# Performance work log

Hardware: AMD Instinct MI355X
Metric: run time of the kernel (lower is better)

## Reference

```python
import jax, jax.numpy as jnp
import numpy as np

B, C, N, H = 4, 256, 1024, 8
D = C // H
EPS = 1e-5

def setup_inputs() -> dict:
    key = jax.random.key(0)
    ks = jax.random.split(key, 10)
    s = lambda k, shape: (jax.random.normal(k, shape, jnp.float32) * 0.02)
    return dict(
        node_embeds=jax.random.normal(ks[0], (B, C, N), jnp.float32),
        edge_embeds=jax.random.normal(ks[1], (B, N, N), jnp.float32),
        da_prior=jax.random.normal(ks[2], (B, N, C), jnp.float32),
        gamma=jnp.ones((C,), jnp.float32),
        beta=jnp.zeros((C,), jnp.float32),
        w_qkv=s(ks[3], (C, 3 * C)),            # Linear(node_dim, 3*node_dim), no bias
        w_proj=s(ks[4], (C, C)),
        b_proj=jnp.zeros((C,), jnp.float32),
        w_expand=s(ks[5], (H,)),               # Conv2d(1,H,1) weight (per-head scalar)
        b_expand=jnp.zeros((H,), jnp.float32),
        w_reduce=s(ks[6], (H,)),               # Conv2d(H,1,1) weight
        b_reduce=jnp.zeros((1,), jnp.float32),
        w_fc=s(ks[7], (1, C)),                 # Linear(edge_dim=1, node_dim)
        b_fc=jnp.zeros((C,), jnp.float32),
    )

def reference(node_embeds, edge_embeds, da_prior, gamma, beta, w_qkv,
              w_proj, b_proj, w_expand, b_expand, w_reduce, b_reduce, w_fc, b_fc):
    x = jnp.swapaxes(node_embeds, 1, 2)                       # [B,N,C]
    # einsum 'bnn,bnc->bnc': diagonal of edge matrix scales each node
    diag = jnp.diagonal(edge_embeds, axis1=1, axis2=2)        # [B,N]
    attned = diag[:, :, None] * x                             # [B,N,C]
    # einsum 'bnc,bca->bnc' with prior permuted [B,C,A]: multiply by sum over A
    prior_sum = da_prior.sum(axis=1)                          # [B,C]
    x = attned * prior_sum[:, None, :] + x                    # residual add
    # LayerNorm over channel dim
    mu = x.mean(-1, keepdims=True)
    var = x.var(-1, keepdims=True)
    ln = (x - mu) * jax.lax.rsqrt(var + EPS) * gamma + beta
    qkv = (ln @ w_qkv).reshape(B, N, 3, H, D)
    q = jnp.transpose(qkv[:, :, 0], (0, 2, 1, 3))             # [B,H,N,D]
    k = jnp.transpose(qkv[:, :, 1], (0, 2, 1, 3))
    v = jnp.transpose(qkv[:, :, 2], (0, 2, 1, 3))
    scale = D ** -0.5
    attn = jnp.einsum('bhnd,bhmd->bhnm', q, k) * scale        # [B,H,N,N]
    bias = edge_embeds[:, None] * w_expand[None, :, None, None] + b_expand[None, :, None, None]
    attn = attn + bias                                        # pre-softmax scores = residual
    a = jax.nn.softmax(attn, axis=-1)
    node = jnp.einsum('bhnm,bhmd->bnhd', a, v).reshape(B, N, C)
    # reduce conv over heads on (softmax + residual)
    edge = jnp.einsum('bhnm,h->bnm', a + attn, w_reduce) + b_reduce[0]  # [B,N,N]
    w = jax.nn.softmax(edge, axis=-1)
    wsum = (w * edge).sum(-1)                                 # [B,N]
    node = node + wsum[:, :, None] @ w_fc + b_fc              # fc: [B,N,1]@[1,C]
    node = node @ w_proj + b_proj
    return jnp.swapaxes(node, 1, 2), edge                     # ([B,C,N], [B,N,N])
```

## Files before the change

kernel.cpp:

```cpp
#include <hip/hip_runtime.h>
#include <math.h>

#define Bn 4
#define Cn 256
#define Nn 1024
#define Hn 8
#define Dn 32
#define BHND (Bn * Hn * Nn * Dn)
#define BHN  (Bn * Hn * Nn)

typedef short bf16x8 __attribute__((ext_vector_type(8)));
typedef float f32x4 __attribute__((ext_vector_type(4)));

__device__ inline unsigned f2bf_rn_bits(float x) {
  union { float f; unsigned u; } v; v.f = x;
  return (v.u + 0x7FFFu + ((v.u >> 16) & 1u)) >> 16;
}
__device__ inline float bfbits2f(unsigned b) {
  union { unsigned u; float f; } v; v.u = b << 16; return v.f;
}
__device__ inline void split_bf(float x, unsigned& hi, unsigned& lo) {
  hi = f2bf_rn_bits(x);
  lo = f2bf_rn_bits(x - bfbits2f(hi));
}
__device__ inline unsigned split_bf_trunc_pack(float x) {
  union { float f; unsigned u; } v; v.f = x;
  unsigned hi = v.u >> 16;
  union { unsigned u; float f; } hv; hv.u = hi << 16;
  union { float f; unsigned u; } r; r.f = x - hv.f;
  return hi | (r.u & 0xffff0000u);
}
__device__ inline void split4(const float4& a, float sc, short4& hs, short4& ls) {
  unsigned hb, lb;
  split_bf(a.x * sc, hb, lb); hs.x = (short)hb; ls.x = (short)lb;
  split_bf(a.y * sc, hb, lb); hs.y = (short)hb; ls.y = (short)lb;
  split_bf(a.z * sc, hb, lb); hs.z = (short)hb; ls.z = (short)lb;
  split_bf(a.w * sc, hb, lb); hs.w = (short)hb; ls.w = (short)lb;
}
__device__ inline void unpack_u32x8(const uint4& a, const uint4& b, bf16x8& hi, bf16x8& lo) {
  int4 h4, l4;
  h4.x = (int)((a.x & 0xffffu) | (a.y << 16));  l4.x = (int)((a.x >> 16) | (a.y & 0xffff0000u));
  h4.y = (int)((a.z & 0xffffu) | (a.w << 16));  l4.y = (int)((a.z >> 16) | (a.w & 0xffff0000u));
  h4.z = (int)((b.x & 0xffffu) | (b.y << 16));  l4.z = (int)((b.x >> 16) | (b.y & 0xffff0000u));
  h4.w = (int)((b.z & 0xffffu) | (b.w << 16));  l4.w = (int)((b.z >> 16) | (b.w & 0xffff0000u));
  hi = *(bf16x8*)&h4; lo = *(bf16x8*)&l4;
}

__global__ __launch_bounds__(256) void k_prior_part(const float* __restrict__ dap,
                                                    float* __restrict__ pp) {
  int bi = blockIdx.x;
  int b = bi >> 5, ch = bi & 31;
  int c = threadIdx.x;
  float s = 0.f;
  int n0 = ch * 32;
  for (int n = n0; n < n0 + 32; ++n) s += dap[(size_t)(b * Nn + n) * Cn + c];
  pp[(size_t)(b * 32 + ch) * Cn + c] = s;
}

__global__ __launch_bounds__(256) void k_prior_red(const float* __restrict__ pp,
                                                   float* __restrict__ prior) {
  int i = blockIdx.x * 256 + threadIdx.x;
  int b = i >> 8, c = i & 255;
  float s = 0.f;
  for (int ch = 0; ch < 32; ++ch) s += pp[(size_t)(b * 32 + ch) * Cn + c];
  prior[i] = s;
}

__global__ __launch_bounds__(256) void k_prep_ln(const float* __restrict__ ne,
                                                 const float* __restrict__ eg,
                                                 const float* __restrict__ prior,
                                                 const float* __restrict__ gamma,
                                                 const float* __restrict__ beta,
                                                 float* __restrict__ ln) {
  int blk = blockIdx.x;
  int xcd = blk & 7, idx = blk >> 3;
  int b = idx >> 7;
  int n = xcd * 128 + (idx & 127);
  int c = threadIdx.x;
  float x = ne[(size_t)(b * Cn + c) * Nn + n];
  float dg = eg[(size_t)(b * Nn + n) * Nn + n];
  float x2 = x * (1.f + dg * prior[b * Cn + c]);
  float s = x2, qq = x2 * x2;
#pragma unroll
  for (int off = 32; off >= 1; off >>= 1) {
    s += __shfl_xor(s, off);
    qq += __shfl_xor(qq, off);
  }
  __shared__ float ss[4], sq[4];
  if ((c & 63) == 0) { ss[c >> 6] = s; sq[c >> 6] = qq; }
  __syncthreads();
  s = ss[0] + ss[1] + ss[2] + ss[3];
  qq = sq[0] + sq[1] + sq[2] + sq[3];
  float mu = s * (1.f / 256.f);
  float var = qq * (1.f / 256.f) - mu * mu;
  float r = rsqrtf(var + 1e-5f);
  ln[(size_t)(b * Nn + n) * Cn + c] = (x2 - mu) * r * gamma[c] + beta[c];
}

__global__ __launch_bounds__(256) void k_qkv_gemm(const float* __restrict__ ln,
                                                  const float* __restrict__ wqkv,
                                                  short* __restrict__ q_hi,
                                                  short* __restrict__ q_lo,
                                                  short* __restrict__ k_hi,
                                                  short* __restrict__ k_lo,
                                                  short* __restrict__ vt_hi,
                                                  short* __restrict__ vt_lo) {
  __shared__ __align__(16) float at[16][68];
  __shared__ __align__(16) float bt[16][68];
  __shared__ float ct[64][65];
  int m0 = blockIdx.x * 64;
  int j0 = blockIdx.y * 64;
  int t = threadIdx.x;
  int tx = t & 15, ty = t >> 4;
  float4 acc[4] = {};
  for (int k0 = 0; k0 < 256; k0 += 16) {
    {
      int row = t >> 2, k4 = (t & 3) << 2;
      float4 a = *(const float4*)&ln[(size_t)(m0 + row) * 256 + k0 + k4];
      at[k4 + 0][row] = a.x; at[k4 + 1][row] = a.y;
      at[k4 + 2][row] = a.z; at[k4 + 3][row] = a.w;
      int rb = t >> 4, jb = (t & 15) << 2;
      *(float4*)&bt[rb][jb] = *(const float4*)&wqkv[(size_t)(k0 + rb) * 768 + j0 + jb];
    }
    __syncthreads();
#pragma unroll
    for (int kk = 0; kk < 16; ++kk) {
      float4 a4 = *(float4*)&at[kk][ty << 2];
      float4 b4 = *(float4*)&bt[kk][tx << 2];
      acc[0].x += a4.x * b4.x; acc[0].y += a4.x * b4.y; acc[0].z += a4.x * b4.z; acc[0].w += a4.x * b4.w;
      acc[1].x += a4.y * b4.x; acc[1].y += a4.y * b4.y; acc[1].z += a4.y * b4.z; acc[1].w += a4.y * b4.w;
      acc[2].x += a4.z * b4.x; acc[2].y += a4.z * b4.y; acc[2].z += a4.z * b4.z; acc[2].w += a4.z * b4.w;
      acc[3].x += a4.w * b4.x; acc[3].y += a4.w * b4.y; acc[3].z += a4.w * b4.z; acc[3].w += a4.w * b4.w;
    }
    __syncthreads();
  }
  int b = m0 >> 10, n0 = m0 & 1023;
  int three = (j0 + (tx << 2)) >> 8;
  const float scale = 0.17677669529663687f;
  if (three == 2) {
#pragma unroll
    for (int i = 0; i < 4; ++i) {
      ct[(ty << 2) + i][(tx << 2) + 0] = acc[i].x;
      ct[(ty << 2) + i][(tx << 2) + 1] = acc[i].y;
      ct[(ty << 2) + i][(tx << 2) + 2] = acc[i].z;
      ct[(ty << 2) + i][(tx << 2) + 3] = acc[i].w;
    }
    __syncthreads();
    int jl = t >> 2;
    int n4 = (t & 3) * 16;
    int rem = (j0 & 255) + jl;
    int h = rem >> 5, d = rem & 31;
    short hs[16], ls[16];
#pragma unroll
    for (int u = 0; u < 16; ++u) {
      unsigned hb, lb;
      split_bf(ct[n4 + u][jl], hb, lb);
      hs[u] = (short)hb; ls[u] = (short)lb;
    }
    size_t ob = ((size_t)(b * Hn + h) * Dn + d) * Nn + n0 + n4;
    *(uint4*)&vt_hi[ob] = *(uint4*)&hs[0];
    *(uint4*)&vt_hi[ob + 8] = *(uint4*)&hs[8];
    *(uint4*)&vt_lo[ob] = *(uint4*)&ls[0];
    *(uint4*)&vt_lo[ob + 8] = *(uint4*)&ls[8];
  } else {
    int j = j0 + (tx << 2);
    int rem = j & 255, h = rem >> 5, dd = rem & 31;
    short* dst_hi = (three == 0) ? q_hi : k_hi;
    short* dst_lo = (three == 0) ? q_lo : k_lo;
    float sc = (three == 0) ? 1.0f : scale;
#pragma unroll
    for (int i = 0; i < 4; ++i) {
      int m = m0 + (ty << 2) + i;
      int bb = m >> 10, n = m & 1023;
      size_t base = (size_t)((bb * Hn + h) * Nn + n) * Dn + dd;
      short4 hs, ls; split4(acc[i], sc, hs, ls);
      *(short4*)&dst_hi[base] = hs; *(short4*)&dst_lo[base] = ls;
    }
  }
}

__global__ __launch_bounds__(256, 4) void k_attn_core(
    const short* __restrict__ q_hi, const short* __restrict__ q_lo,
    const short* __restrict__ k_hi, const short* __restrict__ k_lo,
    const short* __restrict__ vt_hi, const short* __restrict__ vt_lo,
    const float* __restrict__ eg,
    const float* __restrict__ w_expand, const float* __restrict__ b_expand,
    float* __restrict__ o_part, float* __restrict__ l_part) {
  __shared__ short kh[64 * 40];
  __shared__ short kl[64 * 40];
  __shared__ short vth[32 * 72];
  __shared__ short vtl[32 * 72];
  __shared__ unsigned pbuf[4][16 * 68];

  int blk = blockIdx.x;
  int mh = blk & 1;
  int nt = (blk >> 1) & 15;
  int h = (blk >> 5) & 7;
  int b = blk >> 8;
  int n0 = nt * 64;
  int t = threadIdx.x, wid = t >> 6, l = t & 63;
  int lr = l & 15, lq = l >> 4;

  const float we = w_expand[h], be = b_expand[h];
  size_t bhb = (size_t)(b * Hn + h) * Nn * Dn;
  const short* khg = k_hi + bhb;
  const short* klg = k_lo + bhb;
  const short* vhg = vt_hi + bhb;
  const short* vlg = vt_lo + bhb;

  bf16x8 qhi, qlo;
  {
    size_t qoff = bhb + (size_t)(n0 + wid * 16 + lr) * Dn + lq * 8;
    qhi = *(const bf16x8*)&q_hi[qoff];
    qlo = *(const bf16x8*)&q_lo[qoff];
  }

  f32x4 O0 = {0.f, 0.f, 0.f, 0.f}, O1 = {0.f, 0.f, 0.f, 0.f};
  float rowsum[4] = {0.f, 0.f, 0.f, 0.f};
  int nrow = n0 + wid * 16 + lq * 4;

  for (int ms = 0; ms < 8; ++ms) {
    int m0 = mh * 512 + ms * 64;
    float eb[4][4];
#pragma unroll
    for (int reg = 0; reg < 4; ++reg) {
      const float* ep = &eg[(size_t)(b * Nn + nrow + reg) * Nn + m0 + lr];
#pragma unroll
      for (int msub = 0; msub < 4; ++msub) eb[msub][reg] = ep[msub * 16];
    }
    __syncthreads();
    {
      int row = t >> 2, c = (t & 3) * 8;
      *(uint4*)&kh[row * 40 + c] = *(const uint4*)&khg[(size_t)(m0 + row) * Dn + c];
      *(uint4*)&kl[row * 40 + c] = *(const uint4*)&klg[(size_t)(m0 + row) * Dn + c];
      int d = t >> 3, cm = (t & 7) * 8;
      *(uint4*)&vth[d * 72 + cm] = *(const uint4*)&vhg[(size_t)d * Nn + m0 + cm];
      *(uint4*)&vtl[d * 72 + cm] = *(const uint4*)&vlg[(size_t)d * Nn + m0 + cm];
    }
    __syncthreads();

#pragma unroll
    for (int msub = 0; msub < 4; ++msub) {
      int mrow = msub * 16 + lr;
      bf16x8 bh8 = *(bf16x8*)&kh[mrow * 40 + lq * 8];
      bf16x8 bl8 = *(bf16x8*)&kl[mrow * 40 + lq * 8];
      f32x4 sacc = {0.f, 0.f, 0.f, 0.f};
      sacc = __builtin_amdgcn_mfma_f32_16x16x32_bf16(qlo, bh8, sacc, 0, 0, 0);
      sacc = __builtin_amdgcn_mfma_f32_16x16x32_bf16(qhi, bl8, sacc, 0, 0, 0);
      sacc = __builtin_amdgcn_mfma_f32_16x16x32_bf16(qhi, bh8, sacc, 0, 0, 0);
#pragma unroll
      for (int reg = 0; reg < 4; ++reg) {
        float s = sacc[reg] + eb[msub][reg] * we + be;
        float e = __expf(s);
        rowsum[reg] += e;
        pbuf[wid][(lq * 4 + reg) * 68 + msub * 16 + lr] = split_bf_trunc_pack(e);
      }
    }

#pragma unroll
    for (int mw = 0; mw < 2; ++mw) {
      uint4 pa = *(uint4*)&pbuf[wid][lr * 68 + mw * 32 + lq * 8];
      uint4 pb = *(uint4*)&pbuf[wid][lr * 68 + mw * 32 + lq * 8 + 4];
      bf16x8 ahi, alo;
      unpack_u32x8(pa, pb, ahi, alo);
      {
        bf16x8 vh8 = *(bf16x8*)&vth[lr * 72 + mw * 32 + lq * 8];
        bf16x8 vl8 = *(bf16x8*)&vtl[lr * 72 + mw * 32 + lq * 8];
        O0 = __builtin_amdgcn_mfma_f32_16x16x32_bf16(alo, vh8, O0, 0, 0, 0);
        O0 = __builtin_amdgcn_mfma_f32_16x16x32_bf16(ahi, vl8, O0, 0, 0, 0);
        O0 = __builtin_amdgcn_mfma_f32_16x16x32_bf16(ahi, vh8, O0, 0, 0, 0);
      }
      {
        bf16x8 vh8 = *(bf16x8*)&vth[(16 + lr) * 72 + mw * 32 + lq * 8];
        bf16x8 vl8 = *(bf16x8*)&vtl[(16 + lr) * 72 + mw * 32 + lq * 8];
        O1 = __builtin_amdgcn_mfma_f32_16x16x32_bf16(alo, vh8, O1, 0, 0, 0);
        O1 = __builtin_amdgcn_mfma_f32_16x16x32_bf16(ahi, vl8, O1, 0, 0, 0);
        O1 = __builtin_amdgcn_mfma_f32_16x16x32_bf16(ahi, vh8, O1, 0, 0, 0);
      }
    }
  }

#pragma unroll
  for (int reg = 0; reg < 4; ++reg) {
#pragma unroll
    for (int off = 1; off < 16; off <<= 1)
      rowsum[reg] += __shfl_xor(rowsum[reg], off);
  }
  size_t pbase = (size_t)mh * BHND + bhb;
#pragma unroll
  for (int reg = 0; reg < 4; ++reg) {
    int n = nrow + reg;
    o_part[pbase + (size_t)n * Dn + lr] = O0[reg];
    o_part[pbase + (size_t)n * Dn + 16 + lr] = O1[reg];
    if (lr == 0)
      l_part[(size_t)mh * BHN + (size_t)(b * Hn + h) * Nn + n] = rowsum[reg];
  }
}

__global__ __launch_bounds__(256, 4) void k_edge_mfma(
    const short* __restrict__ q_hi, const short* __restrict__ q_lo,
    const short* __restrict__ k_hi, const short* __restrict__ k_lo,
    const float* __restrict__ eg, const float* __restrict__ l_part,
    const float* __restrict__ w_expand, const float* __restrict__ b_expand,
    const float* __restrict__ w_reduce, const float* __restrict__ b_reduce,
    float* __restrict__ edge_out) {
  __shared__ short kh[64 * 40];
  __shared__ short kl[64 * 40];
  int blk = blockIdx.x;
  int mt = blk & 15;
  int nt = (blk >> 4) & 15;
  int b = blk >> 8;
  int n0 = nt * 64, m0 = mt * 64;
  int t = threadIdx.x, wid = t >> 6, l = t & 63;
  int lr = l & 15, lq = l >> 4;
  const float br = b_reduce[0];
  int nrow = n0 + wid * 16 + lq * 4;

  float eacc[4][4], ebias[4][4];
#pragma unroll
  for (int reg = 0; reg < 4; ++reg) {
    const float* ep = &eg[(size_t)(b * Nn + nrow + reg) * Nn + m0 + lr];
#pragma unroll
    for (int msub = 0; msub < 4; ++msub) {
      ebias[msub][reg] = ep[msub * 16];
      eacc[msub][reg] = br;
    }
  }

  for (int h = 0; h < Hn; ++h) {
    size_t bhb = (size_t)(b * Hn + h) * Nn * Dn;
    float we = w_expand[h], be = b_expand[h], wr = w_reduce[h];
    bf16x8 qhi, qlo;
    {
      size_t qoff = bhb + (size_t)(n0 + wid * 16 + lr) * Dn + lq * 8;
      qhi = *(const bf16x8*)&q_hi[qoff];
      qlo = *(const bf16x8*)&q_lo[qoff];
    }
    float invl[4];
#pragma unroll
    for (int reg = 0; reg < 4; ++reg) {
      size_t sidx = (size_t)(b * Hn + h) * Nn + nrow + reg;
      invl[reg] = 1.0f / (l_part[sidx] + l_part[BHN + sidx]);
    }

    __syncthreads();
    {
      int row = t >> 2, c = (t & 3) * 8;
      *(uint4*)&kh[row * 40 + c] = *(const uint4*)&k_hi[bhb + (size_t)(m0 + row) * Dn + c];
      *(uint4*)&kl[row * 40 + c] = *(const uint4*)&k_lo[bhb + (size_t)(m0 + row) * Dn + c];
    }
    __syncthreads();
#pragma unroll
    for (int msub = 0; msub < 4; ++msub) {
      int mrow = msub * 16 + lr;
      bf16x8 bh8 = *(bf16x8*)&kh[mrow * 40 + lq * 8];
      bf16x8 bl8 = *(bf16x8*)&kl[mrow * 40 + lq * 8];
      f32x4 sacc = {0.f, 0.f, 0.f, 0.f};
      sacc = __builtin_amdgcn_mfma_f32_16x16x32_bf16(qlo, bh8, sacc, 0, 0, 0);
      sacc = __builtin_amdgcn_mfma_f32_16x16x32_bf16(qhi, bl8, sacc, 0, 0, 0);
      sacc = __builtin_amdgcn_mfma_f32_16x16x32_bf16(qhi, bh8, sacc, 0, 0, 0);
#pragma unroll
      for (int reg = 0; reg < 4; ++reg) {
        float s = sacc[reg] + ebias[msub][reg] * we + be;
        float p = __expf(s) * invl[reg];
        eacc[msub][reg] += wr * (p + s);
      }
    }
  }
#pragma unroll
  for (int msub = 0; msub < 4; ++msub)
#pragma unroll
    for (int reg = 0; reg < 4; ++reg)
      edge_out[(size_t)(b * Nn + nrow + reg) * Nn + m0 + msub * 16 + lr] = eacc[msub][reg];
}

__global__ __launch_bounds__(256) void k_edge_soft(const float* __restrict__ edge,
                                                   float* __restrict__ wsum) {
  int bn = blockIdx.x;
  int t = threadIdx.x;
  const float* row = edge + (size_t)bn * Nn;
  float4 e = *(const float4*)&row[t * 4];
  float mx = fmaxf(fmaxf(e.x, e.y), fmaxf(e.z, e.w));
#pragma unroll
  for (int off = 32; off >= 1; off >>= 1) mx = fmaxf(mx, __shfl_xor(mx, off));
  __shared__ float sm[4], sl[4], sw[4];
  if ((t & 63) == 0) sm[t >> 6] = mx;
  __syncthreads();
  mx = fmaxf(fmaxf(sm[0], sm[1]), fmaxf(sm[2], sm[3]));
  float p0 = __expf(e.x - mx), p1 = __expf(e.y - mx), p2 = __expf(e.z - mx), p3 = __expf(e.w - mx);
  float ls = p0 + p1 + p2 + p3;
  float ws = p0 * e.x + p1 * e.y + p2 * e.z + p3 * e.w;
#pragma unroll
  for (int off = 32; off >= 1; off >>= 1) { ls += __shfl_xor(ls, off); ws += __shfl_xor(ws, off); }
  if ((t & 63) == 0) { sl[t >> 6] = ls; sw[t >> 6] = ws; }
  __syncthreads();
  if (t == 0) {
    float L = sl[0] + sl[1] + sl[2] + sl[3];
    float Wv = sw[0] + sw[1] + sw[2] + sw[3];
    wsum[bn] = Wv / L;
  }
}

__global__ __launch_bounds__(256) void k_proj_gemm(const float* __restrict__ o_part,
                                                   const float* __restrict__ l_part,
                                                   const float* __restrict__ wsum,
                                                   const float* __restrict__ wfc,
                                                   const float* __restrict__ bfc,
                                                   const float* __restrict__ wproj,
                                                   const float* __restrict__ bproj,
                                                   float* __restrict__ out) {
  __shared__ __align__(16) float at[16][68];
  __shared__ __align__(16) float bt[16][68];
  __shared__ float ct[64][65];
  int m0 = blockIdx.x * 64;
  int j0 = blockIdx.y * 64;
  int t = threadIdx.x;
  int tx = t & 15, ty = t >> 4;
  float4 acc[4] = {};
  for (int k0 = 0; k0 < 256; k0 += 16) {
    {
      int row = t >> 2, k4 = (t & 3) << 2;
      int m = m0 + row;
      int bb = m >> 10, n = m & 1023;
      int c = k0 + k4;
      int h = c >> 5, dd = c & 31;
      float wsm = wsum[m];
      size_t ob = ((size_t)(bb * Hn + h) * Nn + n) * Dn + dd;
      float4 oa = *(const float4*)&o_part[ob];
      float4 oc = *(const float4*)&o_part[BHND + ob];
      size_t sidx = (size_t)(bb * Hn + h) * Nn + n;
      float inv = 1.0f / (l_part[sidx] + l_part[BHN + sidx]);
      float4 a;
      a.x = (oa.x + oc.x) * inv + wsm * wfc[c + 0] + bfc[c + 0];
      a.y = (oa.y + oc.y) * inv + wsm * wfc[c + 1] + bfc[c + 1];
      a.z = (oa.z + oc.z) * inv + wsm * wfc[c + 2] + bfc[c + 2];
      a.w = (oa.w + oc.w) * inv + wsm * wfc[c + 3] + bfc[c + 3];
      at[k4 + 0][row] = a.x; at[k4 + 1][row] = a.y;
      at[k4 + 2][row] = a.z; at[k4 + 3][row] = a.w;
      int rb = t >> 4, jb = (t & 15) << 2;
      *(float4*)&bt[rb][jb] = *(const float4*)&wproj[(size_t)(k0 + rb) * 256 + j0 + jb];
    }
    __syncthreads();
#pragma unroll
    for (int kk = 0; kk < 16; ++kk) {
      float4 a4 = *(float4*)&at[kk][ty << 2];
      float4 b4 = *(float4*)&bt[kk][tx << 2];
      acc[0].x += a4.x * b4.x; acc[0].y += a4.x * b4.y; acc[0].z += a4.x * b4.z; acc[0].w += a4.x * b4.w;
      acc[1].x += a4.y * b4.x; acc[1].y += a4.y * b4.y; acc[1].z += a4.y * b4.z; acc[1].w += a4.y * b4.w;
      acc[2].x += a4.z * b4.x; acc[2].y += a4.z * b4.y; acc[2].z += a4.z * b4.z; acc[2].w += a4.z * b4.w;
      acc[3].x += a4.w * b4.x; acc[3].y += a4.w * b4.y; acc[3].z += a4.w * b4.z; acc[3].w += a4.w * b4.w;
    }
    __syncthreads();
  }
#pragma unroll
  for (int i = 0; i < 4; ++i) {
    ct[(ty << 2) + i][(tx << 2) + 0] = acc[i].x + bproj[j0 + (tx << 2) + 0];
    ct[(ty << 2) + i][(tx << 2) + 1] = acc[i].y + bproj[j0 + (tx << 2) + 1];
    ct[(ty << 2) + i][(tx << 2) + 2] = acc[i].z + bproj[j0 + (tx << 2) + 2];
    ct[(ty << 2) + i][(tx << 2) + 3] = acc[i].w + bproj[j0 + (tx << 2) + 3];
  }
  __syncthreads();
  int b = m0 >> 10, n0 = m0 & 1023;
  int n4 = t & 15, c0i = t >> 4;
#pragma unroll
  for (int u = 0; u < 4; ++u) {
    int ci = c0i + u * 16;
    float4 val = { ct[(n4 << 2) + 0][ci], ct[(n4 << 2) + 1][ci],
                   ct[(n4 << 2) + 2][ci], ct[(n4 << 2) + 3][ci] };
    *(float4*)&out[(size_t)(b * Cn + j0 + ci) * Nn + n0 + (n4 << 2)] = val;
  }
}

extern "C" void kernel_launch(void* const* d_in, const int* in_sizes, int n_in,
                              void* d_out, int out_size, void* d_ws, size_t ws_size,
                              hipStream_t stream) {
  (void)in_sizes; (void)n_in; (void)out_size; (void)ws_size;
  const float* node_embeds = (const float*)d_in[0];
  const float* edge_embeds = (const float*)d_in[1];
  const float* da_prior    = (const float*)d_in[2];
  const float* gamma       = (const float*)d_in[3];
  const float* beta        = (const float*)d_in[4];
  const float* w_qkv       = (const float*)d_in[5];
  const float* w_proj      = (const float*)d_in[6];
  const float* b_proj      = (const float*)d_in[7];
  const float* w_expand    = (const float*)d_in[8];
  const float* b_expand    = (const float*)d_in[9];
  const float* w_reduce    = (const float*)d_in[10];
  const float* b_reduce    = (const float*)d_in[11];
  const float* w_fc        = (const float*)d_in[12];
  const float* b_fc        = (const float*)d_in[13];
  float* out_node = (float*)d_out;
  float* out_edge = out_node + (size_t)Bn * Cn * Nn;

  const size_t M = 1048576;
  float* W = (float*)d_ws;
  float* o_part = W;
  float* ws_ln  = W + M;
  short* vt_hi  = (short*)(W + 2 * M);
  short* vt_lo  = vt_hi + M;
  short* q_hi   = (short*)(W + 3 * M);
  short* q_lo   = q_hi + M;
  short* k_hi   = q_hi + 2 * M;
  short* k_lo   = q_hi + 3 * M;
  float* ws_pp    = W + 5 * M;
  float* ws_prior = ws_pp + Bn * 32 * Cn;
  float* ws_wsum  = ws_prior + Bn * Cn;
  float* l_part   = ws_wsum + Bn * Nn;

  k_prior_part<<<dim3(Bn * 32), dim3(256), 0, stream>>>(da_prior, ws_pp);
  k_prior_red<<<dim3(Bn), dim3(256), 0, stream>>>(ws_pp, ws_prior);
  k_prep_ln<<<dim3(Bn * Nn), dim3(256), 0, stream>>>(node_embeds, edge_embeds,
                                                     ws_prior, gamma, beta, ws_ln);
  k_qkv_gemm<<<dim3(64, 12), dim3(256), 0, stream>>>(ws_ln, w_qkv, q_hi, q_lo,
                                                     k_hi, k_lo, vt_hi, vt_lo);
  k_attn_core<<<dim3(Bn * Hn * 16 * 2), dim3(256), 0, stream>>>(
      q_hi, q_lo, k_hi, k_lo, vt_hi, vt_lo, edge_embeds, w_expand, b_expand,
      o_part, l_part);
  k_edge_mfma<<<dim3(Bn * 16 * 16), dim3(256), 0, stream>>>(
      q_hi, q_lo, k_hi, k_lo, edge_embeds, l_part, w_expand, b_expand,
      w_reduce, b_reduce, out_edge);
  k_edge_soft<<<dim3(Bn * Nn), dim3(256), 0, stream>>>(out_edge, ws_wsum);
  k_proj_gemm<<<dim3(64, 4), dim3(256), 0, stream>>>(o_part, l_part, ws_wsum,
                                                     w_fc, b_fc, w_proj, b_proj,
                                                     out_node);
}
```

Measured before the change: 201.3 us.

## Double query rows per attention block and split keys four ways

Each k_attn_core block now handles 128 query rows (two 64-row groups) against a quarter of the keys, instead of 64 rows against half. Each K/V tile staged in shared memory is reused by twice as many query rows, halving K/V global loads per unit of work, and the grid stays at 1024 blocks. In exchange there are four partial O/l buffers, so the edge and projection kernels read and sum four partials, which adds memory traffic and workspace. Register pressure also grows from the doubled accumulators and bias arrays.

```diff
diff --git a/kernel.cpp b/kernel.cpp
--- a/kernel.cpp
+++ b/kernel.cpp
@@ -193,11 +193,11 @@
   __shared__ unsigned pbuf[4][16 * 68];
 
   int blk = blockIdx.x;
-  int mh = blk & 1;
-  int nt = (blk >> 1) & 15;
+  int mh = blk & 3;
+  int nt = (blk >> 2) & 7;
   int h = (blk >> 5) & 7;
   int b = blk >> 8;
-  int n0 = nt * 64;
+  int n0 = nt * 128;
   int t = threadIdx.x, wid = t >> 6, l = t & 63;
   int lr = l & 15, lq = l >> 4;
 
@@ -208,25 +208,27 @@
   const short* vhg = vt_hi + bhb;
   const short* vlg = vt_lo + bhb;
 
-  bf16x8 qhi, qlo;
-  {
-    size_t qoff = bhb + (size_t)(n0 + wid * 16 + lr) * Dn + lq * 8;
-    qhi = *(const bf16x8*)&q_hi[qoff];
-    qlo = *(const bf16x8*)&q_lo[qoff];
-  }
-
-  f32x4 O0 = {0.f, 0.f, 0.f, 0.f}, O1 = {0.f, 0.f, 0.f, 0.f};
-  float rowsum[4] = {0.f, 0.f, 0.f, 0.f};
-  int nrow = n0 + wid * 16 + lq * 4;
-
-  for (int ms = 0; ms < 8; ++ms) {
-    int m0 = mh * 512 + ms * 64;
-    float eb[4][4];
+  bf16x8 qh[2], ql[2];
+#pragma unroll
+  for (int rg = 0; rg < 2; ++rg) {
+    size_t qoff = bhb + (size_t)(n0 + rg * 64 + wid * 16 + lr) * Dn + lq * 8;
+    qh[rg] = *(const bf16x8*)&q_hi[qoff];
+    ql[rg] = *(const bf16x8*)&q_lo[qoff];
+  }
+
+  f32x4 O[2][2] = {{{0.f,0.f,0.f,0.f},{0.f,0.f,0.f,0.f}},
+                   {{0.f,0.f,0.f,0.f},{0.f,0.f,0.f,0.f}}};
+  float rowsum[2][4] = {{0.f,0.f,0.f,0.f},{0.f,0.f,0.f,0.f}};
+  int nrowb[2] = {n0 + wid * 16 + lq * 4, n0 + 64 + wid * 16 + lq * 4};
+
+  for (int ms = 0; ms < 4; ++ms) {
+    int m0 = mh * 256 + ms * 64;
+    float eb0[4][4];
 #pragma unroll
     for (int reg = 0; reg < 4; ++reg) {
-      const float* ep = &eg[(size_t)(b * Nn + nrow + reg) * Nn + m0 + lr];
-#pragma unroll
-      for (int msub = 0; msub < 4; ++msub) eb[msub][reg] = ep[msub * 16];
+      const float* ep = &eg[(size_t)(b * Nn + nrowb[0] + reg) * Nn + m0 + lr];
+#pragma unroll
+      for (int msub = 0; msub < 4; ++msub) eb0[msub][reg] = ep[msub * 16];
     }
     __syncthreads();
     {
@@ -238,63 +240,77 @@
       *(uint4*)&vtl[d * 72 + cm] = *(const uint4*)&vlg[(size_t)d * Nn + m0 + cm];
     }
     __syncthreads();
-
-#pragma unroll
-    for (int msub = 0; msub < 4; ++msub) {
-      int mrow = msub * 16 + lr;
-      bf16x8 bh8 = *(bf16x8*)&kh[mrow * 40 + lq * 8];
-      bf16x8 bl8 = *(bf16x8*)&kl[mrow * 40 + lq * 8];
-      f32x4 sacc = {0.f, 0.f, 0.f, 0.f};
-      sacc = __builtin_amdgcn_mfma_f32_16x16x32_bf16(qlo, bh8, sacc, 0, 0, 0);
-      sacc = __builtin_amdgcn_mfma_f32_16x16x32_bf16(qhi, bl8, sacc, 0, 0, 0);
-      sacc = __builtin_amdgcn_mfma_f32_16x16x32_bf16(qhi, bh8, sacc, 0, 0, 0);
-#pragma unroll
-      for (int reg = 0; reg < 4; ++reg) {
-        float s = sacc[reg] + eb[msub][reg] * we + be;
-        float e = __expf(s);
-        rowsum[reg] += e;
-        pbuf[wid][(lq * 4 + reg) * 68 + msub * 16 + lr] = split_bf_trunc_pack(e);
+    float eb1[4][4];
+#pragma unroll
+    for (int reg = 0; reg < 4; ++reg) {
+      const float* ep = &eg[(size_t)(b * Nn + nrowb[1] + reg) * Nn + m0 + lr];
+#pragma unroll
+      for (int msub = 0; msub < 4; ++msub) eb1[msub][reg] = ep[msub * 16];
+    }
+
+#pragma unroll
+    for (int rg = 0; rg < 2; ++rg) {
+#pragma unroll
+      for (int msub = 0; msub < 4; ++msub) {
+        int mrow = msub * 16 + lr;
+        bf16x8 bh8 = *(bf16x8*)&kh[mrow * 40 + lq * 8];
+        bf16x8 bl8 = *(bf16x8*)&kl[mrow * 40 + lq * 8];
+        f32x4 sacc = {0.f, 0.f, 0.f, 0.f};
+        sacc = __builtin_amdgcn_mfma_f32_16x16x32_bf16(ql[rg], bh8, sacc, 0, 0, 0);
+        sacc = __builtin_amdgcn_mfma_f32_16x16x32_bf16(qh[rg], bl8, sacc, 0, 0, 0);
+        sacc = __builtin_amdgcn_mfma_f32_16x16x32_bf16(qh[rg], bh8, sacc, 0, 0, 0);
+#pragma unroll
+        for (int reg = 0; reg < 4; ++reg) {
+          float bias = (rg == 0 ? eb0[msub][reg] : eb1[msub][reg]) * we + be;
+          float s = sacc[reg] + bias;
+          float e = __expf(s);
+          rowsum[rg][reg] += e;
+          pbuf[wid][(lq * 4 + reg) * 68 + msub * 16 + lr] = split_bf_trunc_pack(e);
+        }
       }
-    }
-
-#pragma unroll
-    for (int mw = 0; mw < 2; ++mw) {
-      uint4 pa = *(uint4*)&pbuf[wid][lr * 68 + mw * 32 + lq * 8];
-      uint4 pb = *(uint4*)&pbuf[wid][lr * 68 + mw * 32 + lq * 8 + 4];
-      bf16x8 ahi, alo;
-      unpack_u32x8(pa, pb, ahi, alo);
-      {
-        bf16x8 vh8 = *(bf16x8*)&vth[lr * 72 + mw * 32 + lq * 8];
-        bf16x8 vl8 = *(bf16x8*)&vtl[lr * 72 + mw * 32 + lq * 8];
-        O0 = __builtin_amdgcn_mfma_f32_16x16x32_bf16(alo, vh8, O0, 0, 0, 0);
-        O0 = __builtin_amdgcn_mfma_f32_16x16x32_bf16(ahi, vl8, O0, 0, 0, 0);
-        O0 = __builtin_amdgcn_mfma_f32_16x16x32_bf16(ahi, vh8, O0, 0, 0, 0);
+#pragma unroll
+      for (int mw = 0; mw < 2; ++mw) {
+        uint4 pa = *(uint4*)&pbuf[wid][lr * 68 + mw * 32 + lq * 8];
+        uint4 pb = *(uint4*)&pbuf[wid][lr * 68 + mw * 32 + lq * 8 + 4];
+        bf16x8 ahi, alo;
+        unpack_u32x8(pa, pb, ahi, alo);
+        {
+          bf16x8 vh8 = *(bf16x8*)&vth[lr * 72 + mw * 32 + lq * 8];
+          bf16x8 vl8 = *(bf16x8*)&vtl[lr * 72 + mw * 32 + lq * 8];
+          O[rg][0] = __builtin_amdgcn_mfma_f32_16x16x32_bf16(alo, vh8, O[rg][0], 0, 0, 0);
+          O[rg][0] = __builtin_amdgcn_mfma_f32_16x16x32_bf16(ahi, vl8, O[rg][0], 0, 0, 0);
+          O[rg][0] = __builtin_amdgcn_mfma_f32_16x16x32_bf16(ahi, vh8, O[rg][0], 0, 0, 0);
+        }
+        {
+          bf16x8 vh8 = *(bf16x8*)&vth[(16 + lr) * 72 + mw * 32 + lq * 8];
+          bf16x8 vl8 = *(bf16x8*)&vtl[(16 + lr) * 72 + mw * 32 + lq * 8];
+          O[rg][1] = __builtin_amdgcn_mfma_f32_16x16x32_bf16(alo, vh8, O[rg][1], 0, 0, 0);
+          O[rg][1] = __builtin_amdgcn_mfma_f32_16x16x32_bf16(ahi, vl8, O[rg][1], 0, 0, 0);
+          O[rg][1] = __builtin_amdgcn_mfma_f32_16x16x32_bf16(ahi, vh8, O[rg][1], 0, 0, 0);
+        }
       }
-      {
-        bf16x8 vh8 = *(bf16x8*)&vth[(16 + lr) * 72 + mw * 32 + lq * 8];
-        bf16x8 vl8 = *(bf16x8*)&vtl[(16 + lr) * 72 + mw * 32 + lq * 8];
-        O1 = __builtin_amdgcn_mfma_f32_16x16x32_bf16(alo, vh8, O1, 0, 0, 0);
-        O1 = __builtin_amdgcn_mfma_f32_16x16x32_bf16(ahi, vl8, O1, 0, 0, 0);
-        O1 = __builtin_amdgcn_mfma_f32_16x16x32_bf16(ahi, vh8, O1, 0, 0, 0);
-      }
-    }
-  }
-
-#pragma unroll
-  for (int reg = 0; reg < 4; ++reg) {
-#pragma unroll
-    for (int off = 1; off < 16; off <<= 1)
-      rowsum[reg] += __shfl_xor(rowsum[reg], off);
-  }
+    }
+  }
+
+#pragma unroll
+  for (int rg = 0; rg < 2; ++rg)
+#pragma unroll
+    for (int reg = 0; reg < 4; ++reg) {
+#pragma unroll
+      for (int off = 1; off < 16; off <<= 1)
+        rowsum[rg][reg] += __shfl_xor(rowsum[rg][reg], off);
+    }
   size_t pbase = (size_t)mh * BHND + bhb;
 #pragma unroll
-  for (int reg = 0; reg < 4; ++reg) {
-    int n = nrow + reg;
-    o_part[pbase + (size_t)n * Dn + lr] = O0[reg];
-    o_part[pbase + (size_t)n * Dn + 16 + lr] = O1[reg];
-    if (lr == 0)
-      l_part[(size_t)mh * BHN + (size_t)(b * Hn + h) * Nn + n] = rowsum[reg];
-  }
+  for (int rg = 0; rg < 2; ++rg)
+#pragma unroll
+    for (int reg = 0; reg < 4; ++reg) {
+      int n = nrowb[rg] + reg;
+      o_part[pbase + (size_t)n * Dn + lr] = O[rg][0][reg];
+      o_part[pbase + (size_t)n * Dn + 16 + lr] = O[rg][1][reg];
+      if (lr == 0)
+        l_part[(size_t)mh * BHN + (size_t)(b * Hn + h) * Nn + n] = rowsum[rg][reg];
+    }
 }
 
 __global__ __launch_bounds__(256, 4) void k_edge_mfma(
@@ -340,7 +356,8 @@
 #pragma unroll
     for (int reg = 0; reg < 4; ++reg) {
       size_t sidx = (size_t)(b * Hn + h) * Nn + nrow + reg;
-      invl[reg] = 1.0f / (l_part[sidx] + l_part[BHN + sidx]);
+      invl[reg] = 1.0f / (l_part[sidx] + l_part[BHN + sidx] +
+                          l_part[2 * BHN + sidx] + l_part[3 * BHN + sidx]);
     }
 
     __syncthreads();
@@ -427,14 +444,17 @@
       float wsm = wsum[m];
       size_t ob = ((size_t)(bb * Hn + h) * Nn + n) * Dn + dd;
       float4 oa = *(const float4*)&o_part[ob];
-      float4 oc = *(const float4*)&o_part[BHND + ob];
+      float4 o1 = *(const float4*)&o_part[BHND + ob];
+      float4 o2 = *(const float4*)&o_part[2 * (size_t)BHND + ob];
+      float4 o3 = *(const float4*)&o_part[3 * (size_t)BHND + ob];
       size_t sidx = (size_t)(bb * Hn + h) * Nn + n;
-      float inv = 1.0f / (l_part[sidx] + l_part[BHN + sidx]);
+      float inv = 1.0f / (l_part[sidx] + l_part[BHN + sidx] +
+                          l_part[2 * BHN + sidx] + l_part[3 * BHN + sidx]);
       float4 a;
-      a.x = (oa.x + oc.x) * inv + wsm * wfc[c + 0] + bfc[c + 0];
-      a.y = (oa.y + oc.y) * inv + wsm * wfc[c + 1] + bfc[c + 1];
-      a.z = (oa.z + oc.z) * inv + wsm * wfc[c + 2] + bfc[c + 2];
-      a.w = (oa.w + oc.w) * inv + wsm * wfc[c + 3] + bfc[c + 3];
+      a.x = (oa.x + o1.x + o2.x + o3.x) * inv + wsm * wfc[c + 0] + bfc[c + 0];
+      a.y = (oa.y + o1.y + o2.y + o3.y) * inv + wsm * wfc[c + 1] + bfc[c + 1];
+      a.z = (oa.z + o1.z + o2.z + o3.z) * inv + wsm * wfc[c + 2] + bfc[c + 2];
+      a.w = (oa.w + o1.w + o2.w + o3.w) * inv + wsm * wfc[c + 3] + bfc[c + 3];
       at[k4 + 0][row] = a.x; at[k4 + 1][row] = a.y;
       at[k4 + 2][row] = a.z; at[k4 + 3][row] = a.w;
       int rb = t >> 4, jb = (t & 15) << 2;
@@ -494,18 +514,18 @@
 
   const size_t M = 1048576;
   float* W = (float*)d_ws;
-  float* o_part = W;
-  float* ws_ln  = W + M;
-  short* vt_hi  = (short*)(W + 2 * M);
+  float* ws_ln  = W;
+  short* vt_hi  = (short*)(W + M);
   short* vt_lo  = vt_hi + M;
-  short* q_hi   = (short*)(W + 3 * M);
+  short* q_hi   = (short*)(W + 2 * M);
   short* q_lo   = q_hi + M;
   short* k_hi   = q_hi + 2 * M;
   short* k_lo   = q_hi + 3 * M;
-  float* ws_pp    = W + 5 * M;
+  float* o_part = W + 4 * M;
+  float* l_part = W + 8 * M;
+  float* ws_pp    = l_part + 4 * BHN;
   float* ws_prior = ws_pp + Bn * 32 * Cn;
   float* ws_wsum  = ws_prior + Bn * Cn;
-  float* l_part   = ws_wsum + Bn * Nn;
 
   k_prior_part<<<dim3(Bn * 32), dim3(256), 0, stream>>>(da_prior, ws_pp);
   k_prior_red<<<dim3(Bn), dim3(256), 0, stream>>>(ws_pp, ws_prior);
@@ -513,7 +533,7 @@
                                                      ws_prior, gamma, beta, ws_ln);
   k_qkv_gemm<<<dim3(64, 12), dim3(256), 0, stream>>>(ws_ln, w_qkv, q_hi, q_lo,
                                                      k_hi, k_lo, vt_hi, vt_lo);
-  k_attn_core<<<dim3(Bn * Hn * 16 * 2), dim3(256), 0, stream>>>(
+  k_attn_core<<<dim3(Bn * Hn * 8 * 4), dim3(256), 0, stream>>>(
       q_hi, q_lo, k_hi, k_lo, vt_hi, vt_lo, edge_embeds, w_expand, b_expand,
       o_part, l_part);
   k_edge_mfma<<<dim3(Bn * 16 * 16), dim3(256), 0, stream>>>(
```

Measured after the change: 201.9 us. No clear change (+0.3%).
